# Optimization experiments

Hardware: AMD Instinct MI355X
Metric: run time of the kernel (lower is better)

The kernel has to match this reference:

```python
import jax, jax.numpy as jnp
import numpy as np

PH, PW = 2, 2
SCALE = (0.5, 0.5)
HARDNESS = 2.0
BN_EPS = 1e-5

def conv2d(x, w, b, pad):
    y = jax.lax.conv_general_dilated(x, w, (1, 1), [(pad, pad), (pad, pad)],
                                     dimension_numbers=('NCHW', 'OIHW', 'NCHW'))
    return y + b[None, :, None, None]

def nearest_resize(x, oh, ow):
    # torch F.interpolate default 'nearest': src_idx = floor(dst_idx * in/out)
    _, _, ih, iw = x.shape
    hi = jnp.floor(jnp.arange(oh) * (ih / oh)).astype(jnp.int32)
    wi = jnp.floor(jnp.arange(ow) * (iw / ow)).astype(jnp.int32)
    return x[:, :, hi][:, :, :, wi]

def bilinear_resize(x, oh, ow):
    # matches torch bilinear align_corners=False (half-pixel, no antialias)
    b, c = x.shape[0], x.shape[1]
    return jax.image.resize(x, (b, c, oh, ow), method='linear', antialias=False)

def grid_sample_bilinear(feat, grid):
    # feat [B,C,H,W], grid [B,gh,gw,2] with (x,y) in [-1,1]; align_corners=False, zeros padding
    B, C, H, W = feat.shape
    gx, gy = grid[..., 0], grid[..., 1]
    ix = (gx + 1.0) * (W * 0.5) - 0.5
    iy = (gy + 1.0) * (H * 0.5) - 0.5
    x0f = jnp.floor(ix); y0f = jnp.floor(iy)
    wx = ix - x0f; wy = iy - y0f
    x0 = x0f.astype(jnp.int32); y0 = y0f.astype(jnp.int32)
    x1 = x0 + 1; y1 = y0 + 1

    def gather(f, yy, xx):
        valid = ((yy >= 0) & (yy < H) & (xx >= 0) & (xx < W)).astype(f.dtype)
        yc = jnp.clip(yy, 0, H - 1); xc = jnp.clip(xx, 0, W - 1)
        return f[:, yc, xc] * valid[None]  # [C,gh,gw]

    def per_sample(f, y0, x0, y1, x1, wx, wy):
        v00 = gather(f, y0, x0); v01 = gather(f, y0, x1)
        v10 = gather(f, y1, x0); v11 = gather(f, y1, x1)
        wx_ = wx[None]; wy_ = wy[None]
        return (v00 * (1 - wx_) * (1 - wy_) + v01 * wx_ * (1 - wy_)
                + v10 * (1 - wx_) * wy_ + v11 * wx_ * wy_)

    return jax.vmap(per_sample)(feat, y0, x0, y1, x1, wx, wy)

def lens_forward(feat, w1, b1, gamma, beta, rmean, rvar, w2, b2):
    B, C, H, W = feat.shape
    dh, dw = H // PH, W // PW
    dsz_h, dsz_w = int(H * SCALE[0]), int(W * SCALE[1])
    # ekern: conv3x3 + BN(eval) + ReLU6
    x = conv2d(feat, w1, b1, 1)
    inv = jax.lax.rsqrt(rvar + BN_EPS)
    x = (x - rmean[None, :, None, None]) * inv[None, :, None, None]
    x = x * gamma[None, :, None, None] + beta[None, :, None, None]
    x = jnp.clip(x, 0.0, 6.0)
    # dkern (eval branch): channel-norm normalize with gating, conv5x5 (no pad) + sigmoid
    nrm = jnp.linalg.norm(x, axis=1, keepdims=True)
    xn = x / (nrm + 9e-8) * (nrm > 0.09).astype(x.dtype)
    dmap_raw = jax.nn.sigmoid(conv2d(xn, w2, b2, 0))  # [B,2,H-4,W-4]
    ndmap = nearest_resize(dmap_raw, dh + 2, dw + 2)
    # dmap += 0.0009; interior += hardness
    mask = jnp.zeros((dh + 2, dw + 2), x.dtype).at[1:-1, 1:-1].set(1.0)
    dmap = ndmap + 0.0009 + HARDNESS * mask[None, None]
    # bilinear round trip through dsz
    dsm = bilinear_resize(dmap, dsz_h, dsz_w)
    dmap = bilinear_resize(dsm, dh + 2, dw + 2)
    # neko_dense_norm: normalize, cumsum -> CDF sampling grid in [-1,1]
    h_ = dmap[:, 0:1]; w_ = dmap[:, 1:2]
    h_ = h_ / jnp.sum(h_, axis=2, keepdims=True)
    w_ = w_ / jnp.sum(w_, axis=3, keepdims=True)
    hc = jnp.cumsum(h_, axis=2); wc = jnp.cumsum(w_, axis=3)
    grid = jnp.concatenate([wc[:, :, 1:-1, 1:-1], hc[:, :, 1:-1, 1:-1]], axis=1) * 2 - 1
    grid = jnp.transpose(grid, (0, 2, 3, 1))  # [B,dh,dw,2] (x,y)
    dst = grid_sample_bilinear(feat, grid)  # [B,C,dh,dw]
    # adaptive_avg_pool2d([dh,dw]) on a [dh,dw] map is identity -> skip
    return dst, dmap

def setup_inputs() -> dict:
    key = jax.random.key(0)
    ks = jax.random.split(key, 9)
    B, ICH, H, W, CH = 16, 64, 256, 256, 64
    feat = jax.random.normal(ks[0], (B, ICH, H, W), jnp.float32)
    w1 = jax.random.normal(ks[1], (CH, ICH, 3, 3), jnp.float32) * 0.05
    b1 = jax.random.normal(ks[2], (CH,), jnp.float32) * 0.05
    gamma = 1.0 + jax.random.normal(ks[3], (CH,), jnp.float32) * 0.05
    beta = jax.random.normal(ks[4], (CH,), jnp.float32) * 0.05
    rmean = jax.random.normal(ks[5], (CH,), jnp.float32) * 0.05
    rvar = jax.random.uniform(ks[6], (CH,), jnp.float32) + 0.5
    w2 = jax.random.normal(ks[7], (2, CH, 5, 5), jnp.float32) * 0.05
    b2 = jax.random.normal(ks[8], (2,), jnp.float32) * 0.05
    return {'feat': feat, 'w1': w1, 'b1': b1, 'gamma': gamma, 'beta': beta,
            'rmean': rmean, 'rvar': rvar, 'w2': w2, 'b2': b2}

def reference(feat, w1, b1, gamma, beta, rmean, rvar, w2, b2):
    dst, dmap = lens_forward(feat, w1, b1, gamma, beta, rmean, rvar, w2, b2)
    return dst, jax.lax.stop_gradient(dmap)
```

## Files before the change

kernel.cpp:

```cpp
#include <hip/hip_runtime.h>
#include <hip/hip_bf16.h>

typedef __hip_bfloat16 bf16;
typedef __attribute__((ext_vector_type(8))) short bf16x8;
typedef __attribute__((ext_vector_type(4))) float f32x4;

static __device__ __forceinline__ ushort f2bf(float f) {
    uint u = __float_as_uint(f);
    u += 0x7fff + ((u >> 16) & 1);
    return (ushort)(u >> 16);
}

static __device__ __forceinline__ void gl_lds16(const void* g, void* l) {
    __builtin_amdgcn_global_load_lds(
        (const __attribute__((address_space(1))) uint*)g,
        (__attribute__((address_space(3))) uint*)l, 16, 0, 0);
}

static __device__ __forceinline__ int xcd_remap(int lid, int nwg) {
    int q = nwg >> 3, r = nwg & 7;
    int xcd = lid & 7, idx = lid >> 3;
    return (xcd < r ? xcd * (q + 1) : r * (q + 1) + (xcd - r) * q) + idx;
}

#define FT_ROW 264
#define FT_IMG ((size_t)258 * 264 * 64)
#define XN_IMG ((size_t)256 * 256 * 64)

__global__ __launch_bounds__(256) void k_wt(const float* __restrict__ w1,
                                            ushort* __restrict__ w_bf) {
    int i = blockIdx.x * 256 + threadIdx.x;
    if (i >= 36864) return;
    int oc = i / 576, rem = i - oc * 576;
    int ic = rem / 9, tap = rem - ic * 9;
    w_bf[tap * 4096 + oc * 64 + (ic ^ ((oc & 7) << 3))] = f2bf(w1[i]);
}

__global__ __launch_bounds__(256) void k_wt2(const float* __restrict__ w2,
                                             ushort* __restrict__ w2_bf) {
    int i = blockIdx.x * 256 + threadIdx.x;
    if (i >= 3200) return;
    int oc = i / 1600, rem = i - oc * 1600;
    int ic = rem / 25, tap = rem - ic * 25;
    w2_bf[(tap * 2 + oc) * 64 + ic] = f2bf(w2[i]);
}

__global__ __launch_bounds__(256) void k_zero(ushort* __restrict__ featT, int nb) {
    int t = blockIdx.x * 256 + threadIdx.x;
    const int per = 1040 * 8;
    if (t >= nb * per) return;
    int b = t / per, u = t - b * per;
    int px = u >> 3, oct = u & 7;
    int yp, xp;
    if (px < 264)       { yp = 0;   xp = px; }
    else if (px < 528)  { yp = 257; xp = px - 264; }
    else { int k = px - 528; yp = 1 + (k >> 1); xp = (k & 1) ? 257 : 0; }
    ushort* p = featT + (size_t)b * FT_IMG + ((size_t)yp * FT_ROW + xp) * 64 + oct * 8;
    *(uint4*)p = make_uint4(0u, 0u, 0u, 0u);
}

__global__ __launch_bounds__(256) void k_tr(const float* __restrict__ feat_c,
                                            ushort* __restrict__ featT) {
    __shared__ ushort s_t[64][72];
    const int b = blockIdx.z, y = blockIdx.y, x0 = blockIdx.x * 64;
    const int t = threadIdx.x;
    const int xl = t & 63, icg = t >> 6;

    const float* fb = feat_c + (size_t)b * 64 * 65536 + (size_t)y * 256 + x0 + xl;
#pragma unroll
    for (int k = 0; k < 16; ++k) {
        int ic = icg * 16 + k;
        s_t[ic][xl] = f2bf(fb[(size_t)ic * 65536]);
    }
    __syncthreads();

    ushort* ob = featT + (size_t)b * FT_IMG + ((size_t)(y + 1) * FT_ROW + (x0 + 1)) * 64;
#pragma unroll
    for (int u2 = 0; u2 < 2; ++u2) {
        int u = u2 * 256 + t;
        int x = u >> 3, oct = u & 7;
        int xp7 = (x + 1) & 7;
        uint p0 = (uint)s_t[oct * 8 + 0][x] | ((uint)s_t[oct * 8 + 1][x] << 16);
        uint p1 = (uint)s_t[oct * 8 + 2][x] | ((uint)s_t[oct * 8 + 3][x] << 16);
        uint p2 = (uint)s_t[oct * 8 + 4][x] | ((uint)s_t[oct * 8 + 5][x] << 16);
        uint p3 = (uint)s_t[oct * 8 + 6][x] | ((uint)s_t[oct * 8 + 7][x] << 16);
        *(uint4*)(ob + (size_t)x * 64 + (oct ^ xp7) * 8) = make_uint4(p0, p1, p2, p3);
    }
}

__global__ __launch_bounds__(256, 2) void k_conv1(
    const ushort* __restrict__ featT, const ushort* __restrict__ w_bf,
    const float* __restrict__ b1, const float* __restrict__ gamma,
    const float* __restrict__ beta, const float* __restrict__ rmean,
    const float* __restrict__ rvar, ushort* __restrict__ xn) {
    __shared__ __align__(16) ushort s_in[6 * 72 * 64];
    __shared__ __align__(16) ushort s_w[12288];
    __shared__ float2 s_bn[64];

    const int lid = blockIdx.x + (blockIdx.y << 2) + (blockIdx.z << 8);
    const int nid = xcd_remap(lid, (int)gridDim.z << 8);
    const int b   = nid >> 8;
    const int x0p = (nid & 3) * 64;
    const int y0  = ((nid >> 2) & 63) * 4;

    const int tid = threadIdx.x;
    const int lane = tid & 63;
    const int w    = tid >> 6;
    const int l15  = lane & 15;
    const int l4   = lane >> 4;

    if (tid < 64) {
        float inv = 1.0f / sqrtf(rvar[tid] + 1e-5f);
        float sA = inv * gamma[tid];
        float sB = (b1[tid] - rmean[tid]) * sA + beta[tid];
        s_bn[tid] = make_float2(sA, sB);
    }

    const ushort* fT = featT + (size_t)b * FT_IMG;
    {
        int aStart = w * 13 + (w < 2 ? w : 2);
        int aCnt   = (w < 2) ? 14 : 13;
        for (int q = 0; q < aCnt; ++q) {
            int o = (aStart + q) * 1024;
            int r = o / 9216;
            int rem = o - r * 9216;
            const ushort* g = fT + ((size_t)(y0 + r) * FT_ROW + x0p) * 64 +
                              (rem >> 1) + lane * 8;
            gl_lds16(g, (char*)s_in + o);
        }
    }

    f32x4 acc[4][4];
#pragma unroll
    for (int m = 0; m < 4; m++)
#pragma unroll
        for (int n = 0; n < 4; n++) acc[m][n] = (f32x4){0.f, 0.f, 0.f, 0.f};

    for (int dy = 0; dy < 3; dy++) {
        __syncthreads();
        {
            for (int q = 0; q < 6; ++q) {
                int o = (w * 6 + q) * 1024;
                const ushort* g = w_bf + dy * 12288 + (o >> 1) + lane * 8;
                gl_lds16(g, (char*)s_w + o);
            }
        }
        __syncthreads();
#pragma unroll
        for (int dx = 0; dx < 3; dx++) {
#pragma unroll
            for (int ks = 0; ks < 2; ks++) {
                bf16x8 a[4], bb[4];
#pragma unroll
                for (int m = 0; m < 4; m++) {
                    int c = m * 16 + l15 + dx;
                    int slot = (ks * 4 + l4) ^ (c & 7);
                    a[m] = *(const bf16x8*)&s_in[((w + dy) * 72 + c) * 64 + slot * 8];
                }
#pragma unroll
                for (int n = 0; n < 4; n++) {
                    int oc = n * 16 + l15;
                    int slot = (ks * 4 + l4) ^ (oc & 7);
                    bb[n] = *(const bf16x8*)&s_w[(dx * 64 + oc) * 64 + slot * 8];
                }
#pragma unroll
                for (int m = 0; m < 4; m++)
#pragma unroll
                    for (int n = 0; n < 4; n++)
                        acc[m][n] = __builtin_amdgcn_mfma_f32_16x16x32_bf16(
                            bb[n], a[m], acc[m][n], 0, 0, 0);
            }
        }
    }

    float sA[4][4], sB[4][4];
#pragma unroll
    for (int n = 0; n < 4; n++)
#pragma unroll
        for (int j = 0; j < 4; j++) {
            float2 t = s_bn[n * 16 + l4 * 4 + j];
            sA[n][j] = t.x; sB[n][j] = t.y;
        }
    const int y = y0 + w;
    ushort* xb = xn + (size_t)b * XN_IMG;

#pragma unroll
    for (int m = 0; m < 4; m++) {
        float vv[4][4];
        float ss = 0.f;
#pragma unroll
        for (int n = 0; n < 4; n++)
#pragma unroll
            for (int j = 0; j < 4; j++) {
                float v = fmaf(acc[m][n][j], sA[n][j], sB[n][j]);
                v = fminf(fmaxf(v, 0.f), 6.f);
                vv[n][j] = v;
                ss = fmaf(v, v, ss);
            }
        ss += __shfl_xor(ss, 16);
        ss += __shfl_xor(ss, 32);
        float nrm = sqrtf(ss);
        float sc = (nrm > 0.09f) ? (1.0f / (nrm + 9e-8f)) : 0.f;

        int x = x0p + m * 16 + l15;
        ushort* pb = xb + ((size_t)y * 256 + x) * 64;
        int so = (l4 & 1) * 4;
#pragma unroll
        for (int n = 0; n < 4; n++) {
            int oct = n * 2 + (l4 >> 1);
            int slot = oct ^ (x & 7);
            uint2 pk;
            pk.x = (uint)f2bf(vv[n][0] * sc) | ((uint)f2bf(vv[n][1] * sc) << 16);
            pk.y = (uint)f2bf(vv[n][2] * sc) | ((uint)f2bf(vv[n][3] * sc) << 16);
            *(uint2*)(pb + slot * 8 + so) = pk;
        }
    }
}

__global__ __launch_bounds__(256, 2) void k_conv2(
    const ushort* __restrict__ xn, const ushort* __restrict__ w2_bf,
    const float* __restrict__ b2, float* __restrict__ dmap_raw) {
    __shared__ __align__(16) ushort s_in[8 * 72 * 64];

    const int lid = blockIdx.x + (blockIdx.y << 2) + blockIdx.z * 252;
    const int nid = xcd_remap(lid, (int)gridDim.z * 252);
    const int b   = nid / 252;
    const int rem = nid - b * 252;
    const int x0  = (rem & 3) * 64;
    const int oy0 = (rem >> 2) * 4;

    const int tid = threadIdx.x;
    const int lane = tid & 63;
    const int w    = tid >> 6;
    const int l15  = lane & 15;
    const int l4   = lane >> 4;

    const ushort* xb = xn + (size_t)b * XN_IMG;
    for (int qq = 0; qq < 18; ++qq) {
        int q = w * 18 + qq;
        int r = q / 9, off = q - r * 9;
        const ushort* g = xb + ((size_t)(oy0 + r) * 256 + x0) * 64 +
                          off * 512 + lane * 8;
        gl_lds16(g, (char*)s_in + q * 1024);
    }
    __syncthreads();

    f32x4 acc[4];
#pragma unroll
    for (int n = 0; n < 4; n++) acc[n] = (f32x4){0.f, 0.f, 0.f, 0.f};

    for (int dy = 0; dy < 5; dy++) {
#pragma unroll
        for (int dx = 0; dx < 5; dx++) {
#pragma unroll
            for (int ks = 0; ks < 2; ks++) {
                bf16x8 aw;
                if (l15 < 2)
                    aw = *(const bf16x8*)(w2_bf + ((dy * 5 + dx) * 2 + l15) * 64 +
                                          ks * 32 + l4 * 8);
                else
                    aw = (bf16x8){0, 0, 0, 0, 0, 0, 0, 0};
                bf16x8 bx[4];
#pragma unroll
                for (int n = 0; n < 4; n++) {
                    int px = n * 16 + l15 + dx;
                    int slot = (ks * 4 + l4) ^ (px & 7);
                    bx[n] = *(const bf16x8*)&s_in[((w + dy) * 72 + px) * 64 + slot * 8];
                }
#pragma unroll
                for (int n = 0; n < 4; n++)
                    acc[n] = __builtin_amdgcn_mfma_f32_16x16x32_bf16(
                        aw, bx[n], acc[n], 0, 0, 0);
            }
        }
    }

    if (l4 == 0) {
        const int oy = oy0 + w;
        float bias0 = b2[0], bias1 = b2[1];
#pragma unroll
        for (int n = 0; n < 4; n++) {
            int ox = x0 + n * 16 + l15;
            if (ox < 252) {
                float v0 = acc[n][0] + bias0;
                float v1 = acc[n][1] + bias1;
                size_t o = (size_t)(b * 2) * 63504 + (size_t)oy * 252 + ox;
                dmap_raw[o] = 1.f / (1.f + expf(-v0));
                dmap_raw[o + 63504] = 1.f / (1.f + expf(-v1));
            }
        }
    }
}

__global__ __launch_bounds__(256) void k_nearest(const float* __restrict__ dmap_raw,
                                                 float* __restrict__ dmapA,
                                                 int total) {
    int i = blockIdx.x * 256 + threadIdx.x;
    if (i >= total) return;
    int ox = i % 130;
    int t = i / 130;
    int oy = t % 130;
    int bc = t / 130;
    const float SC = (float)(252.0 / 130.0);
    int sy = (int)floorf((float)oy * SC);
    int sx = (int)floorf((float)ox * SC);
    float v = dmap_raw[(size_t)bc * 63504 + sy * 252 + sx];
    float m = (oy >= 1 && oy <= 128 && ox >= 1 && ox <= 128) ? 2.0f : 0.0f;
    dmapA[i] = v + 0.0009f + m;
}

__global__ __launch_bounds__(256) void k_bilinear(const float* __restrict__ in,
                                                  float* __restrict__ out,
                                                  int IH, int IW, int OH, int OW,
                                                  float sch, float scw, int total) {
    int i = blockIdx.x * 256 + threadIdx.x;
    if (i >= total) return;
    int ox = i % OW;
    int t = i / OW;
    int oy = t % OH;
    int bc = t / OH;
    float sy = ((float)oy + 0.5f) * sch - 0.5f;
    float sx = ((float)ox + 0.5f) * scw - 0.5f;
    float y0f = floorf(sy), x0f = floorf(sx);
    float wy = sy - y0f, wx = sx - x0f;
    int y0 = (int)y0f, x0 = (int)x0f;
    int y1 = y0 + 1, x1 = x0 + 1;
    y0 = max(min(y0, IH - 1), 0);
    y1 = max(min(y1, IH - 1), 0);
    x0 = max(min(x0, IW - 1), 0);
    x1 = max(min(x1, IW - 1), 0);
    const float* p = in + (size_t)bc * IH * IW;
    float top = p[y0 * IW + x0] * (1.f - wx) + p[y0 * IW + x1] * wx;
    float bot = p[y1 * IW + x0] * (1.f - wx) + p[y1 * IW + x1] * wx;
    out[i] = top * (1.f - wy) + bot * wy;
}

__global__ __launch_bounds__(256) void k_grid(const float* __restrict__ dmap130,
                                              float* __restrict__ grid) {
    int b = blockIdx.x;
    int t = threadIdx.x;
    if (t >= 130) return;
    const float* h = dmap130 + (size_t)(b * 2 + 0) * 16900;
    const float* w = dmap130 + (size_t)(b * 2 + 1) * 16900;
    float* g = grid + (size_t)b * 128 * 128 * 2;

    {
        float s = 0.f;
        for (int r = 0; r < 130; r++) s += h[r * 130 + t];
        float inv = 1.f / s;
        float c = 0.f;
        for (int r = 0; r < 130; r++) {
            c += h[r * 130 + t] * inv;
            if (r >= 1 && r <= 128 && t >= 1 && t <= 128)
                g[((r - 1) * 128 + (t - 1)) * 2 + 1] = c * 2.f - 1.f;
        }
    }
    {
        const float* wrow = w + t * 130;
        float s = 0.f;
        for (int x = 0; x < 130; x++) s += wrow[x];
        float inv = 1.f / s;
        float c = 0.f;
        for (int x = 0; x < 130; x++) {
            c += wrow[x] * inv;
            if (x >= 1 && x <= 128 && t >= 1 && t <= 128)
                g[((t - 1) * 128 + (x - 1)) * 2 + 0] = c * 2.f - 1.f;
        }
    }
}

__global__ __launch_bounds__(256) void k_sample(const float* __restrict__ feat_c,
                                                const float* __restrict__ grid,
                                                float* __restrict__ dst_c) {
    const int b = blockIdx.z;
    const int x = blockIdx.x * 16 + (threadIdx.x & 15);
    const int y = blockIdx.y * 16 + (threadIdx.x >> 4);

    const float* g = grid + (((size_t)b * 128 + y) * 128 + x) * 2;
    float gx = g[0], gy = g[1];
    float ix = (gx + 1.f) * 128.f - 0.5f;
    float iy = (gy + 1.f) * 128.f - 0.5f;
    float x0f = floorf(ix), y0f = floorf(iy);
    float wx = ix - x0f, wy = iy - y0f;
    int ix0 = (int)x0f, iy0 = (int)y0f;
    int ix1 = ix0 + 1, iy1 = iy0 + 1;
    float vx0 = ((unsigned)ix0 < 256u) ? 1.f : 0.f;
    float vx1 = ((unsigned)ix1 < 256u) ? 1.f : 0.f;
    float vy0 = ((unsigned)iy0 < 256u) ? 1.f : 0.f;
    float vy1 = ((unsigned)iy1 < 256u) ? 1.f : 0.f;
    int cx0 = max(min(ix0, 255), 0), cx1 = max(min(ix1, 255), 0);
    int cy0 = max(min(iy0, 255), 0), cy1 = max(min(iy1, 255), 0);
    float w00 = (1.f - wx) * (1.f - wy) * vx0 * vy0;
    float w01 = wx * (1.f - wy) * vx1 * vy0;
    float w10 = (1.f - wx) * wy * vx0 * vy1;
    float w11 = wx * wy * vx1 * vy1;

    const float* fb = feat_c + (size_t)b * 64 * 65536;
    int o00 = cy0 * 256 + cx0, o01 = cy0 * 256 + cx1;
    int o10 = cy1 * 256 + cx0, o11 = cy1 * 256 + cx1;
    float* d = dst_c + (size_t)b * 64 * 16384 + (size_t)y * 128 + x;
#pragma unroll 4
    for (int c = 0; c < 64; c++) {
        const float* fc = fb + (size_t)c * 65536;
        d[(size_t)c * 16384] = fc[o00] * w00 + fc[o01] * w01 +
                               fc[o10] * w10 + fc[o11] * w11;
    }
}

static inline size_t align256(size_t x) { return (x + 255) & ~(size_t)255; }

extern "C" void kernel_launch(void* const* d_in, const int* in_sizes, int n_in,
                              void* d_out, int out_size, void* d_ws, size_t ws_size,
                              hipStream_t stream) {
    const float* feat  = (const float*)d_in[0];
    const float* w1    = (const float*)d_in[1];
    const float* b1    = (const float*)d_in[2];
    const float* gamma = (const float*)d_in[3];
    const float* beta  = (const float*)d_in[4];
    const float* rmean = (const float*)d_in[5];
    const float* rvar  = (const float*)d_in[6];
    const float* w2    = (const float*)d_in[7];
    const float* b2    = (const float*)d_in[8];

    float* out = (float*)d_out;
    float* out_dst  = out;
    float* out_dmap = out + 16777216;

    int nb = 1;
    const int cands[5] = {16, 8, 4, 2, 1};
    for (int k = 0; k < 5; ++k) {
        int n = cands[k];
        size_t need = align256((size_t)n * FT_IMG * 2)
                    + align256((size_t)n * XN_IMG * 2)
                    + align256(73728)
                    + align256(12800)
                    + align256((size_t)n * 2 * 63504 * 4)
                    + align256((size_t)n * 2 * 16900 * 4)
                    + align256((size_t)n * 2 * 16384 * 4)
                    + align256((size_t)n * 131072);
        if (need <= ws_size) { nb = n; break; }
    }

    char* p = (char*)d_ws;
    ushort* featT   = (ushort*)p; p += align256((size_t)nb * FT_IMG * 2);
    ushort* xn      = (ushort*)p; p += align256((size_t)nb * XN_IMG * 2);
    ushort* w_bf    = (ushort*)p; p += align256(73728);
    ushort* w2_bf   = (ushort*)p; p += align256(12800);
    float* dmap_raw = (float*)p;  p += align256((size_t)nb * 2 * 63504 * 4);
    float* dmapA    = (float*)p;  p += align256((size_t)nb * 2 * 16900 * 4);
    float* dsm      = (float*)p;  p += align256((size_t)nb * 2 * 16384 * 4);
    float* grid     = (float*)p;

    k_wt<<<144, 256, 0, stream>>>(w1, w_bf);
    k_wt2<<<13, 256, 0, stream>>>(w2, w2_bf);

    const int nchunks = 16 / nb;
    for (int c = 0; c < nchunks; ++c) {
        const float* feat_c = feat + (size_t)c * nb * 64 * 65536;
        float* dst_c  = out_dst  + (size_t)c * nb * 64 * 16384;
        float* dmap_c = out_dmap + (size_t)c * nb * 2 * 16900;

        k_zero<<<(nb * 8320 + 255) / 256, 256, 0, stream>>>(featT, nb);
        k_tr<<<dim3(4, 256, nb), 256, 0, stream>>>(feat_c, featT);
        k_conv1<<<dim3(4, 64, nb), 256, 0, stream>>>(featT, w_bf, b1, gamma,
                                                     beta, rmean, rvar, xn);
        k_conv2<<<dim3(4, 63, nb), 256, 0, stream>>>(xn, w2_bf, b2, dmap_raw);
        k_nearest<<<(nb * 2 * 16900 + 255) / 256, 256, 0, stream>>>(
            dmap_raw, dmapA, nb * 2 * 16900);
        k_bilinear<<<(nb * 2 * 16384 + 255) / 256, 256, 0, stream>>>(
            dmapA, dsm, 130, 130, 128, 128,
            (float)(130.0 / 128.0), (float)(130.0 / 128.0), nb * 2 * 16384);
        k_bilinear<<<(nb * 2 * 16900 + 255) / 256, 256, 0, stream>>>(
            dsm, dmap_c, 128, 128, 130, 130,
            (float)(128.0 / 130.0), (float)(128.0 / 130.0), nb * 2 * 16900);
        k_grid<<<nb, 256, 0, stream>>>(dmap_c, grid);
        k_sample<<<dim3(8, 8, nb), 256, 0, stream>>>(feat_c, grid, dst_c);
    }
}
```

Before: 425.1 us.

## Compute conv2 only on rows sampled by nearest resize and fuse dmap stages

conv2 now evaluates only the 130 output rows that the nearest-neighbor downsample actually reads, instead of all 252 rows, cutting the grid roughly in half. It loads the needed input rows into LDS in two channel halves to fit the smaller buffer. The nearest, two bilinear and grid-cumsum kernels are merged into one kernel per (batch, channel) that keeps intermediates in shared memory. That kernel removes launches and global round trips, but it runs with only 2*nb blocks and large LDS use, so it has low parallelism.

```diff
diff --git a/kernel.cpp b/kernel.cpp
--- a/kernel.cpp
+++ b/kernel.cpp
@@ -219,13 +219,13 @@
 
 __global__ __launch_bounds__(256, 2) void k_conv2(
     const ushort* __restrict__ xn, const ushort* __restrict__ w2_bf,
-    const float* __restrict__ b2, float* __restrict__ dmap_raw) {
-    __shared__ __align__(16) ushort s_in[8 * 72 * 64];
-
-    const int lid = blockIdx.x + (blockIdx.y << 2) + blockIdx.z * 252;
-    const int nid = xcd_remap(lid, (int)gridDim.z * 252);
-    const int b   = nid / 252;
-    const int rem = nid - b * 252;
+    const float* __restrict__ b2, float* __restrict__ dmap_raw2) {
+    __shared__ __align__(16) ushort s_in[11 * 80 * 32];
+
+    const int lid = blockIdx.x + (blockIdx.y << 2) + blockIdx.z * 132;
+    const int nid = xcd_remap(lid, (int)gridDim.z * 132);
+    const int b   = nid / 132;
+    const int rem = nid - b * 132;
     const int x0  = (rem & 3) * 64;
     const int oy0 = (rem >> 2) * 4;
 
@@ -235,37 +235,52 @@
     const int l15  = lane & 15;
     const int l4   = lane >> 4;
 
+    const float SC = (float)(252.0 / 130.0);
+    const int syb = (int)floorf((float)oy0 * SC);
+    const int oy  = oy0 + w;
+    const int syrel = (int)floorf((float)oy * SC) - syb;
+
     const ushort* xb = xn + (size_t)b * XN_IMG;
-    for (int qq = 0; qq < 18; ++qq) {
-        int q = w * 18 + qq;
-        int r = q / 9, off = q - r * 9;
-        const ushort* g = xb + ((size_t)(oy0 + r) * 256 + x0) * 64 +
-                          off * 512 + lane * 8;
-        gl_lds16(g, (char*)s_in + q * 1024);
-    }
-    __syncthreads();
 
     f32x4 acc[4];
 #pragma unroll
     for (int n = 0; n < 4; n++) acc[n] = (f32x4){0.f, 0.f, 0.f, 0.f};
 
-    for (int dy = 0; dy < 5; dy++) {
-#pragma unroll
-        for (int dx = 0; dx < 5; dx++) {
-#pragma unroll
-            for (int ks = 0; ks < 2; ks++) {
+    for (int c = 0; c < 2; ++c) {
+        if (c) __syncthreads();
+        {
+            int st  = (w < 3) ? w * 14 : 42;
+            int cnt = (w < 3) ? 14 : 13;
+            for (int q = 0; q < cnt; ++q) {
+                int i = st + q;
+                int r = i / 5;
+                int px0 = (i - r * 5) * 16;
+                int gr = min(syb + r, 255);
+                int px = px0 + (lane >> 2);
+                int gx = x0 + px;
+                const ushort* g = xb + (size_t)(gr * 256 + gx) * 64 +
+                                  ((((gx >> 2) & 1) ^ c) * 32) + (lane & 3) * 8;
+                gl_lds16(g, (char*)s_in + i * 1024);
+            }
+        }
+        __syncthreads();
+
+#pragma unroll
+        for (int dy = 0; dy < 5; dy++) {
+#pragma unroll
+            for (int dx = 0; dx < 5; dx++) {
                 bf16x8 aw;
                 if (l15 < 2)
                     aw = *(const bf16x8*)(w2_bf + ((dy * 5 + dx) * 2 + l15) * 64 +
-                                          ks * 32 + l4 * 8);
+                                          c * 32 + l4 * 8);
                 else
                     aw = (bf16x8){0, 0, 0, 0, 0, 0, 0, 0};
                 bf16x8 bx[4];
 #pragma unroll
                 for (int n = 0; n < 4; n++) {
                     int px = n * 16 + l15 + dx;
-                    int slot = (ks * 4 + l4) ^ (px & 7);
-                    bx[n] = *(const bf16x8*)&s_in[((w + dy) * 72 + px) * 64 + slot * 8];
+                    int slot4 = l4 ^ (px & 3);
+                    bx[n] = *(const bf16x8*)&s_in[((syrel + dy) * 80 + px) * 32 + slot4 * 8];
                 }
 #pragma unroll
                 for (int n = 0; n < 4; n++)
@@ -275,8 +290,7 @@
         }
     }
 
-    if (l4 == 0) {
-        const int oy = oy0 + w;
+    if (l4 == 0 && oy < 130) {
         float bias0 = b2[0], bias1 = b2[1];
 #pragma unroll
         for (int n = 0; n < 4; n++) {
@@ -284,87 +298,92 @@
             if (ox < 252) {
                 float v0 = acc[n][0] + bias0;
                 float v1 = acc[n][1] + bias1;
-                size_t o = (size_t)(b * 2) * 63504 + (size_t)oy * 252 + ox;
-                dmap_raw[o] = 1.f / (1.f + expf(-v0));
-                dmap_raw[o + 63504] = 1.f / (1.f + expf(-v1));
-            }
-        }
-    }
-}
-
-__global__ __launch_bounds__(256) void k_nearest(const float* __restrict__ dmap_raw,
-                                                 float* __restrict__ dmapA,
-                                                 int total) {
-    int i = blockIdx.x * 256 + threadIdx.x;
-    if (i >= total) return;
-    int ox = i % 130;
-    int t = i / 130;
-    int oy = t % 130;
-    int bc = t / 130;
+                size_t o = (size_t)b * 65520 + (size_t)oy * 252 + ox;
+                dmap_raw2[o] = 1.f / (1.f + expf(-v0));
+                dmap_raw2[o + 32760] = 1.f / (1.f + expf(-v1));
+            }
+        }
+    }
+}
+
+__global__ __launch_bounds__(256) void k_dmap(const float* __restrict__ dmap_raw2,
+                                              float* __restrict__ out_dmap,
+                                              float* __restrict__ grid) {
+    __shared__ float sA[16900];
+    __shared__ float sB[16384];
+    const int ch = blockIdx.x, b = blockIdx.y;
+    const int tid = threadIdx.x;
     const float SC = (float)(252.0 / 130.0);
-    int sy = (int)floorf((float)oy * SC);
-    int sx = (int)floorf((float)ox * SC);
-    float v = dmap_raw[(size_t)bc * 63504 + sy * 252 + sx];
-    float m = (oy >= 1 && oy <= 128 && ox >= 1 && ox <= 128) ? 2.0f : 0.0f;
-    dmapA[i] = v + 0.0009f + m;
-}
-
-__global__ __launch_bounds__(256) void k_bilinear(const float* __restrict__ in,
-                                                  float* __restrict__ out,
-                                                  int IH, int IW, int OH, int OW,
-                                                  float sch, float scw, int total) {
-    int i = blockIdx.x * 256 + threadIdx.x;
-    if (i >= total) return;
-    int ox = i % OW;
-    int t = i / OW;
-    int oy = t % OH;
-    int bc = t / OH;
-    float sy = ((float)oy + 0.5f) * sch - 0.5f;
-    float sx = ((float)ox + 0.5f) * scw - 0.5f;
-    float y0f = floorf(sy), x0f = floorf(sx);
-    float wy = sy - y0f, wx = sx - x0f;
-    int y0 = (int)y0f, x0 = (int)x0f;
-    int y1 = y0 + 1, x1 = x0 + 1;
-    y0 = max(min(y0, IH - 1), 0);
-    y1 = max(min(y1, IH - 1), 0);
-    x0 = max(min(x0, IW - 1), 0);
-    x1 = max(min(x1, IW - 1), 0);
-    const float* p = in + (size_t)bc * IH * IW;
-    float top = p[y0 * IW + x0] * (1.f - wx) + p[y0 * IW + x1] * wx;
-    float bot = p[y1 * IW + x0] * (1.f - wx) + p[y1 * IW + x1] * wx;
-    out[i] = top * (1.f - wy) + bot * wy;
-}
-
-__global__ __launch_bounds__(256) void k_grid(const float* __restrict__ dmap130,
-                                              float* __restrict__ grid) {
-    int b = blockIdx.x;
-    int t = threadIdx.x;
-    if (t >= 130) return;
-    const float* h = dmap130 + (size_t)(b * 2 + 0) * 16900;
-    const float* w = dmap130 + (size_t)(b * 2 + 1) * 16900;
-    float* g = grid + (size_t)b * 128 * 128 * 2;
+
+    const float* src = dmap_raw2 + (size_t)b * 65520 + (size_t)ch * 32760;
+    for (int i = tid; i < 16900; i += 256) {
+        int oy = i / 130, ox = i - oy * 130;
+        int sx = (int)floorf((float)ox * SC);
+        float m = (oy >= 1 && oy <= 128 && ox >= 1 && ox <= 128) ? 2.0f : 0.0f;
+        sA[i] = src[oy * 252 + sx] + 0.0009f + m;
+    }
+    __syncthreads();
 
     {
-        float s = 0.f;
-        for (int r = 0; r < 130; r++) s += h[r * 130 + t];
-        float inv = 1.f / s;
-        float c = 0.f;
-        for (int r = 0; r < 130; r++) {
-            c += h[r * 130 + t] * inv;
-            if (r >= 1 && r <= 128 && t >= 1 && t <= 128)
-                g[((r - 1) * 128 + (t - 1)) * 2 + 1] = c * 2.f - 1.f;
-        }
-    }
+        const float sc = (float)(130.0 / 128.0);
+        for (int i = tid; i < 16384; i += 256) {
+            int oy = i >> 7, ox = i & 127;
+            float sy = ((float)oy + 0.5f) * sc - 0.5f;
+            float sx = ((float)ox + 0.5f) * sc - 0.5f;
+            float y0f = floorf(sy), x0f = floorf(sx);
+            float wy = sy - y0f, wx = sx - x0f;
+            int y0 = max(min((int)y0f, 129), 0), y1 = max(min((int)y0f + 1, 129), 0);
+            int x0 = max(min((int)x0f, 129), 0), x1 = max(min((int)x0f + 1, 129), 0);
+            float top = sA[y0 * 130 + x0] * (1.f - wx) + sA[y0 * 130 + x1] * wx;
+            float bot = sA[y1 * 130 + x0] * (1.f - wx) + sA[y1 * 130 + x1] * wx;
+            sB[i] = top * (1.f - wy) + bot * wy;
+        }
+    }
+    __syncthreads();
+
     {
-        const float* wrow = w + t * 130;
-        float s = 0.f;
-        for (int x = 0; x < 130; x++) s += wrow[x];
-        float inv = 1.f / s;
-        float c = 0.f;
-        for (int x = 0; x < 130; x++) {
-            c += wrow[x] * inv;
-            if (x >= 1 && x <= 128 && t >= 1 && t <= 128)
-                g[((t - 1) * 128 + (x - 1)) * 2 + 0] = c * 2.f - 1.f;
+        const float sc = (float)(128.0 / 130.0);
+        float* od = out_dmap + ((size_t)b * 2 + ch) * 16900;
+        for (int i = tid; i < 16900; i += 256) {
+            int oy = i / 130, ox = i - oy * 130;
+            float sy = ((float)oy + 0.5f) * sc - 0.5f;
+            float sx = ((float)ox + 0.5f) * sc - 0.5f;
+            float y0f = floorf(sy), x0f = floorf(sx);
+            float wy = sy - y0f, wx = sx - x0f;
+            int y0 = max(min((int)y0f, 127), 0), y1 = max(min((int)y0f + 1, 127), 0);
+            int x0 = max(min((int)x0f, 127), 0), x1 = max(min((int)x0f + 1, 127), 0);
+            float top = sB[y0 * 128 + x0] * (1.f - wx) + sB[y0 * 128 + x1] * wx;
+            float bot = sB[y1 * 128 + x0] * (1.f - wx) + sB[y1 * 128 + x1] * wx;
+            float v = top * (1.f - wy) + bot * wy;
+            od[i] = v;
+            sA[i] = v;
+        }
+    }
+    __syncthreads();
+
+    if (tid < 130) {
+        float* g = grid + (size_t)b * 32768;
+        if (ch == 0) {
+            float s = 0.f;
+            for (int r = 0; r < 130; r++) s += sA[r * 130 + tid];
+            float inv = 1.f / s;
+            float cs = 0.f;
+            for (int r = 0; r < 130; r++) {
+                cs += sA[r * 130 + tid] * inv;
+                if (r >= 1 && r <= 128 && tid >= 1 && tid <= 128)
+                    g[((r - 1) * 128 + (tid - 1)) * 2 + 1] = cs * 2.f - 1.f;
+            }
+        } else {
+            const float* row = sA + tid * 130;
+            float s = 0.f;
+            for (int x = 0; x < 130; x++) s += row[x];
+            float inv = 1.f / s;
+            float cs = 0.f;
+            for (int x = 0; x < 130; x++) {
+                cs += row[x] * inv;
+                if (x >= 1 && x <= 128 && tid >= 1 && tid <= 128)
+                    g[((tid - 1) * 128 + (x - 1)) * 2 + 0] = cs * 2.f - 1.f;
+            }
         }
     }
 }
@@ -434,22 +453,18 @@
                     + align256((size_t)n * XN_IMG * 2)
                     + align256(73728)
                     + align256(12800)
-                    + align256((size_t)n * 2 * 63504 * 4)
-                    + align256((size_t)n * 2 * 16900 * 4)
-                    + align256((size_t)n * 2 * 16384 * 4)
+                    + align256((size_t)n * 65520 * 4)
                     + align256((size_t)n * 131072);
         if (need <= ws_size) { nb = n; break; }
     }
 
     char* p = (char*)d_ws;
-    ushort* featT   = (ushort*)p; p += align256((size_t)nb * FT_IMG * 2);
-    ushort* xn      = (ushort*)p; p += align256((size_t)nb * XN_IMG * 2);
-    ushort* w_bf    = (ushort*)p; p += align256(73728);
-    ushort* w2_bf   = (ushort*)p; p += align256(12800);
-    float* dmap_raw = (float*)p;  p += align256((size_t)nb * 2 * 63504 * 4);
-    float* dmapA    = (float*)p;  p += align256((size_t)nb * 2 * 16900 * 4);
-    float* dsm      = (float*)p;  p += align256((size_t)nb * 2 * 16384 * 4);
-    float* grid     = (float*)p;
+    ushort* featT    = (ushort*)p; p += align256((size_t)nb * FT_IMG * 2);
+    ushort* xn       = (ushort*)p; p += align256((size_t)nb * XN_IMG * 2);
+    ushort* w_bf     = (ushort*)p; p += align256(73728);
+    ushort* w2_bf    = (ushort*)p; p += align256(12800);
+    float* dmap_raw2 = (float*)p;  p += align256((size_t)nb * 65520 * 4);
+    float* grid      = (float*)p;
 
     k_wt<<<144, 256, 0, stream>>>(w1, w_bf);
     k_wt2<<<13, 256, 0, stream>>>(w2, w2_bf);
@@ -464,16 +479,8 @@
         k_tr<<<dim3(4, 256, nb), 256, 0, stream>>>(feat_c, featT);
         k_conv1<<<dim3(4, 64, nb), 256, 0, stream>>>(featT, w_bf, b1, gamma,
                                                      beta, rmean, rvar, xn);
-        k_conv2<<<dim3(4, 63, nb), 256, 0, stream>>>(xn, w2_bf, b2, dmap_raw);
-        k_nearest<<<(nb * 2 * 16900 + 255) / 256, 256, 0, stream>>>(
-            dmap_raw, dmapA, nb * 2 * 16900);
-        k_bilinear<<<(nb * 2 * 16384 + 255) / 256, 256, 0, stream>>>(
-            dmapA, dsm, 130, 130, 128, 128,
-            (float)(130.0 / 128.0), (float)(130.0 / 128.0), nb * 2 * 16384);
-        k_bilinear<<<(nb * 2 * 16900 + 255) / 256, 256, 0, stream>>>(
-            dsm, dmap_c, 128, 128, 130, 130,
-            (float)(128.0 / 130.0), (float)(128.0 / 130.0), nb * 2 * 16900);
-        k_grid<<<nb, 256, 0, stream>>>(dmap_c, grid);
+        k_conv2<<<dim3(4, 33, nb), 256, 0, stream>>>(xn, w2_bf, b2, dmap_raw2);
+        k_dmap<<<dim3(2, nb), 256, 0, stream>>>(dmap_raw2, dmap_c, grid);
         k_sample<<<dim3(8, 8, nb), 256, 0, stream>>>(feat_c, grid, dst_c);
     }
 }
```

Result: faster. 407.4 us (-4.2%).
